# Performance work log

Measured on AMD Instinct MI355X. Metric: run time of the kernel, lower is better.

The kernel has to match this reference:

```python
import jax, jax.numpy as jnp
import numpy as np

N = 50000      # n_nodes
E = 800000     # n_edges
D = 64         # in_dim == out_dim
K = 3          # k-neighbourhoods {1,2,3} at t=2
T = 2          # layer index t
NU = 1         # cfg.nu -> delay(k) = max(k - nu, 0)
AGG_EPS = 1e-6
BN_EPS = 1e-5


def setup_inputs() -> dict:
    key = jax.random.key(0)
    ks = jax.random.split(key, 8)
    xs = jax.random.normal(ks[0], (T + 1, N, D), dtype=jnp.float32)
    edge_index = jax.random.randint(ks[1], (2, E), 0, N, dtype=jnp.int32)
    edge_attr = jax.random.randint(ks[2], (E,), 1, K + 1, dtype=jnp.int32)  # hop k in {1..K}
    s = 1.0 / np.sqrt(D)
    Wa = jax.random.normal(ks[3], (D, D), dtype=jnp.float32) * s
    Wd = jax.random.normal(ks[4], (D, D), dtype=jnp.float32) * s
    Wb = jax.random.normal(ks[5], (K, D, D), dtype=jnp.float32) * s
    return {
        "xs": xs,
        "edge_index": edge_index,
        "edge_attr": edge_attr,
        "Wa": Wa, "ba": jnp.zeros((D,), jnp.float32),
        "Wd": Wd, "bd": jnp.zeros((D,), jnp.float32),
        "Wb": Wb, "bb": jnp.zeros((K, D), jnp.float32),
        "gamma": jnp.ones((D,), jnp.float32),
        "beta": jnp.zeros((D,), jnp.float32),
    }


def reference(xs, edge_index, edge_attr, Wa, ba, Wd, bd, Wb, bb, gamma, beta):
    # current node state
    x = xs[T]  # [N, D]
    # delayed state per hop k: xs[t - max(k - nu, 0)] -> indices [2, 1, 0] for k = 1,2,3
    state_idx = jnp.array([T - max(k - NU, 0) for k in range(1, K + 1)])
    states = xs[state_idx]                                   # [K, N, D]
    # per-k linear B_k (source uses B for both Bx and Ex)
    Bx = jnp.einsum('knd,kdo->kno', states, Wb) + bb[:, None, :]  # [K, N, D]
    Ex = Bx
    Ax = x @ Wa + ba                                         # [N, D]
    Dx = x @ Wd + bd                                         # [N, D]

    i_idx = edge_index[1]                                    # destination
    j_idx = edge_index[0]                                    # source
    ke = edge_attr - 1                                       # [E], 0..K-1

    Dx_i = Dx[i_idx]                                         # [E, D]
    Ex_j = Ex[ke, j_idx]                                     # [E, D] per-k gather
    Bx_j = Bx[ke, j_idx]                                     # [E, D]

    sigma = jax.nn.sigmoid(Dx_i + Ex_j)                      # [E, D]

    # per-(node, k) scatter-sum; segment id packs (i, k)
    seg = i_idx * K + ke
    num = jax.ops.segment_sum(sigma * Bx_j, seg, num_segments=N * K).reshape(N, K, D)
    den = jax.ops.segment_sum(sigma, seg, num_segments=N * K).reshape(N, K, D)
    eta = num / (den + AGG_EPS)                              # [N, K, D]

    alpha = 1.0 / K  # softmax(ones(K)) with convex combination
    x_new = Ax + alpha * eta.sum(axis=1)                     # [N, D]

    # BatchNorm1d over nodes (training-mode batch statistics, biased var)
    mean = x_new.mean(axis=0)
    var = jnp.var(x_new, axis=0)
    y = gamma * (x_new - mean) * jax.lax.rsqrt(var + BN_EPS) + beta
    return jax.nn.relu(y)  # dropout p=0.0, residual=False
```

## Files before the change

### kernel.cpp

```cpp
#include <hip/hip_runtime.h>
#include <hip/hip_bf16.h>

#define D 64
#define K 3

typedef __hip_bfloat16 bf16;

__device__ __forceinline__ float b2f(bf16 v) { return __bfloat162float(v); }

__device__ __forceinline__ unsigned short f2bf(float f)
{
    const unsigned x = __float_as_uint(f);
    return (unsigned short)((x + 0x7FFFu + ((x >> 16) & 1u)) >> 16);
}

#define P_WA 0
#define P_BA 4096
#define P_WD 4160
#define P_BD 8256
#define P_WB 8320
#define P_BB 20608
#define P_G  20800
#define P_B  20864
#define P_TOTAL 20928

#define LOG2E 1.442695041f

#define NB_MAX 1024
#define BKN    128
#define BKSEG  (BKN * K)

__global__ void cvt_hist_kernel(const void* Wa, const void* ba, const void* Wd, const void* bd,
                                const void* Wb, const void* bb, const void* g, const void* b,
                                float* __restrict__ P, int* __restrict__ flag,
                                const int* __restrict__ ei,
                                int* __restrict__ bcnt, int E, int HB, int cb, int NB)
{
    __shared__ int bins[NB_MAX];
    const int bid = blockIdx.x;
    const int tid = threadIdx.x;

    if (bid < HB) {
        for (int i = tid; i < NB; i += 256) bins[i] = 0;
        __syncthreads();
        const int tstr = HB * 256;
        for (int e = bid * 256 + tid; e < E; e += tstr)
            atomicAdd(&bins[ei[E + e] >> 7], 1);
        __syncthreads();
        for (int i = tid; i < NB; i += 256) {
            const int c = bins[i];
            if (c) atomicAdd(&bcnt[i], c);
        }
        return;
    }

    const int isbf = (((const unsigned int*)g)[0] == 0x3F803F80u) ? 1 : 0;
    if (bid == HB && tid == 0) *flag = isbf;
    int i = (bid - HB) * 256 + tid;
    const int stride = cb * 256;
    for (; i < P_TOTAL; i += stride) {
        const void* src; int off;
        if (i < P_BA)      { src = Wa; off = i; }
        else if (i < P_WD) { src = ba; off = i - P_BA; }
        else if (i < P_BD) { src = Wd; off = i - P_WD; }
        else if (i < P_WB) { src = bd; off = i - P_BD; }
        else if (i < P_BB) { src = Wb; off = i - P_WB; }
        else if (i < P_G)  { src = bb; off = i - P_BB; }
        else if (i < P_B)  { src = g;  off = i - P_G; }
        else               { src = b;  off = i - P_B; }
        float v;
        if (isbf) v = b2f(((const bf16*)src)[off]);
        else      v = ((const float*)src)[off];
        P[i] = v;
    }
}

union U8 { float4 f; ushort4 u; };

__device__ __forceinline__ void lin_load(U8 reg[8], const void* xs_raw, size_t xbase,
                                         int isbf, int tid, int nbase, int N)
{
    if (isbf) {
        const ushort* xp = (const ushort*)xs_raw + xbase;
        #pragma unroll
        for (int p = 0; p < 8; p++) {
            const int idx = tid + (p << 8);
            const int n = nbase + (idx >> 4), c4 = (idx & 15) << 2;
            if (n < N) reg[p].u = *(const ushort4*)(xp + (size_t)n * D + c4);
            else       reg[p].u = make_ushort4(0, 0, 0, 0);
        }
    } else {
        const float* xp = (const float*)xs_raw + xbase;
        #pragma unroll
        for (int p = 0; p < 8; p++) {
            const int idx = tid + (p << 8);
            const int n = nbase + (idx >> 4), c4 = (idx & 15) << 2;
            if (n < N) reg[p].f = *(const float4*)(xp + (size_t)n * D + c4);
            else       reg[p].f = make_float4(0.f, 0.f, 0.f, 0.f);
        }
    }
}

__global__ void lin_scan_kernel(const void* __restrict__ xs_raw,
                                const float* __restrict__ P, const int* __restrict__ flag,
                                float* __restrict__ Ax, float* __restrict__ Dx,
                                void* __restrict__ Bx, int N,
                                const int* __restrict__ bcnt, int* __restrict__ bbase,
                                int* __restrict__ bcur, int* __restrict__ off,
                                int M, int E, int NB, int gx, int LB)
{
    __shared__ __align__(16) float sw[64][64];
    __shared__ float sx[128][65];
    __shared__ float sbias[64];
    __shared__ int sscan[256];

    const int bid = blockIdx.x;
    const int tid = threadIdx.x;

    if (bid >= LB) {
        const int base = tid * 4;
        int v[4];
        #pragma unroll
        for (int q = 0; q < 4; q++) {
            const int i = base + q;
            v[q] = (i < NB) ? bcnt[i] : 0;
        }
        const int tsum = v[0] + v[1] + v[2] + v[3];
        sscan[tid] = tsum;
        __syncthreads();
        #pragma unroll
        for (int o = 1; o < 256; o <<= 1) {
            int x = (tid >= o) ? sscan[tid - o] : 0;
            __syncthreads();
            sscan[tid] += x;
            __syncthreads();
        }
        int run = sscan[tid] - tsum;
        #pragma unroll
        for (int q = 0; q < 4; q++) {
            const int i = base + q;
            if (i < NB) { bbase[i] = run; bcur[i] = run; }
            run += v[q];
        }
        if (tid == 0) off[M] = E;
        return;
    }

    const int isbf = *flag;
    const int which = bid / gx;
    const int t0    = bid % gx;
    const size_t ND = (size_t)N * D;

    const float* W; const float* bias; size_t xbase;
    float* outf = nullptr; ushort* outh = nullptr;
    if (which == 0)      { W = P + P_WA; bias = P + P_BA; xbase = 2 * ND; outf = Ax; }
    else if (which == 1) { W = P + P_WD; bias = P + P_BD; xbase = 2 * ND; outf = Dx; }
    else {
        const int k = which - 2;
        W = P + P_WB + (size_t)k * D * D;
        bias = P + P_BB + (size_t)k * D;
        const int layer = 2 - k;
        xbase = (size_t)layer * ND;
        if (isbf) outh = (ushort*)Bx + k * ND;
        else      outf = (float*)Bx + k * ND;
    }
    const int bfout = (outh != nullptr);

    for (int idx = tid; idx < D * D; idx += 256)
        sw[idx >> 6][idx & 63] = W[idx];
    if (tid < 64) sbias[tid] = bias[tid];

    const int tiles = (N + 127) >> 7;

    U8 reg[8];
    int t = t0;
    if (t < tiles) lin_load(reg, xs_raw, xbase, isbf, tid, t << 7, N);

    const int ct = tid & 7;  const int c0 = ct * 8;
    const int nt = tid >> 3; const int n0 = nt * 4;

    for (; t < tiles; t += gx) {
        __syncthreads();
        #pragma unroll
        for (int p = 0; p < 8; p++) {
            const int idx = tid + (p << 8);
            const int n = idx >> 4, c4 = (idx & 15) << 2;
            float v0, v1, v2, v3;
            if (isbf) {
                v0 = __uint_as_float((unsigned)reg[p].u.x << 16);
                v1 = __uint_as_float((unsigned)reg[p].u.y << 16);
                v2 = __uint_as_float((unsigned)reg[p].u.z << 16);
                v3 = __uint_as_float((unsigned)reg[p].u.w << 16);
            } else {
                v0 = reg[p].f.x; v1 = reg[p].f.y; v2 = reg[p].f.z; v3 = reg[p].f.w;
            }
            sx[n][c4 + 0] = v0; sx[n][c4 + 1] = v1;
            sx[n][c4 + 2] = v2; sx[n][c4 + 3] = v3;
        }
        __syncthreads();

        const int tn = t + gx;
        if (tn < tiles) lin_load(reg, xs_raw, xbase, isbf, tid, tn << 7, N);

        float acc[4][8];
        {
            float b0[8];
            #pragma unroll
            for (int j = 0; j < 8; j++) b0[j] = sbias[c0 + j];
            #pragma unroll
            for (int i = 0; i < 4; i++)
                #pragma unroll
                for (int j = 0; j < 8; j++) acc[i][j] = b0[j];
        }

        #pragma unroll 8
        for (int kk = 0; kk < 64; kk++) {
            const float4 wlo = *(const float4*)&sw[kk][c0];
            const float4 whi = *(const float4*)&sw[kk][c0 + 4];
            float xv[4];
            #pragma unroll
            for (int i = 0; i < 4; i++) xv[i] = sx[n0 + i][kk];
            #pragma unroll
            for (int i = 0; i < 4; i++) {
                acc[i][0] += xv[i] * wlo.x; acc[i][1] += xv[i] * wlo.y;
                acc[i][2] += xv[i] * wlo.z; acc[i][3] += xv[i] * wlo.w;
                acc[i][4] += xv[i] * whi.x; acc[i][5] += xv[i] * whi.y;
                acc[i][6] += xv[i] * whi.z; acc[i][7] += xv[i] * whi.w;
            }
        }

        const int nbase = t << 7;
        #pragma unroll
        for (int i = 0; i < 4; i++) {
            const int gn = nbase + n0 + i;
            if (gn < N) {
                if (bfout) {
                    ushort* op = outh + (size_t)gn * D + c0;
                    *(ushort4*)op = make_ushort4(f2bf(acc[i][0]), f2bf(acc[i][1]),
                                                 f2bf(acc[i][2]), f2bf(acc[i][3]));
                    *(ushort4*)(op + 4) = make_ushort4(f2bf(acc[i][4]), f2bf(acc[i][5]),
                                                       f2bf(acc[i][6]), f2bf(acc[i][7]));
                } else {
                    float* op = outf + (size_t)gn * D + c0;
                    *(float4*)op       = make_float4(acc[i][0], acc[i][1], acc[i][2], acc[i][3]);
                    *(float4*)(op + 4) = make_float4(acc[i][4], acc[i][5], acc[i][6], acc[i][7]);
                }
            }
        }
    }
}

__global__ void binscat_kernel(const int* __restrict__ ei, const int* __restrict__ ea,
                               int* __restrict__ bcur, int* __restrict__ bkt,
                               int E, int NB, int CH)
{
    __shared__ int lcnt[NB_MAX];
    __shared__ int lbase[NB_MAX];
    const int bid = blockIdx.x, tid = threadIdx.x;
    const int s0 = bid * CH;
    int s1 = s0 + CH; if (s1 > E) s1 = E;

    for (int i = tid; i < NB; i += 256) lcnt[i] = 0;
    __syncthreads();
    for (int e = s0 + tid; e < s1; e += 256)
        atomicAdd(&lcnt[ei[E + e] >> 7], 1);
    __syncthreads();
    for (int b = tid; b < NB; b += 256) {
        const int c = lcnt[b];
        lbase[b] = c ? atomicAdd(&bcur[b], c) : 0;
        lcnt[b] = 0;
    }
    __syncthreads();
    for (int e = s0 + tid; e < s1; e += 256) {
        const int i  = ei[E + e];
        const int j  = ei[e];
        const int ke = ea[e] - 1;
        const int b  = i >> 7;
        const int r  = atomicAdd(&lcnt[b], 1);
        bkt[lbase[b] + r] = ((i & 127) << 19) | (ke << 17) | j;
    }
}

__global__ void bucketsort_kernel(const int* __restrict__ bbase, const int* __restrict__ bcur,
                                  const int* __restrict__ bkt,
                                  int* __restrict__ off, int* __restrict__ elist, int M)
{
    __shared__ int cl[512];
    __shared__ int cu[512];
    const int b = blockIdx.x, tid = threadIdx.x;
    const int s0 = bbase[b], s1 = bcur[b];

    cl[tid] = 0; cl[tid + 256] = 0;
    __syncthreads();
    for (int idx = s0 + tid; idx < s1; idx += 256) {
        const int p = bkt[idx];
        atomicAdd(&cl[(p >> 19) * 3 + ((p >> 17) & 3)], 1);
    }
    __syncthreads();
    const int c0 = cl[tid], c1 = cl[tid + 256];
    for (int o = 1; o < 512; o <<= 1) {
        const int a0 = (tid >= o) ? cl[tid - o] : 0;
        const int a1 = cl[tid + 256 - o];
        __syncthreads();
        cl[tid] += a0; cl[tid + 256] += a1;
        __syncthreads();
    }
    const int e0 = cl[tid] - c0, e1 = cl[tid + 256] - c1;
    cu[tid] = e0; cu[tid + 256] = e1;
    const int gbase = b * BKSEG;
    {
        const int gs0 = gbase + tid;
        if (tid < BKSEG && gs0 < M) off[gs0] = s0 + e0;
        const int ls1 = tid + 256;
        const int gs1 = gbase + ls1;
        if (ls1 < BKSEG && gs1 < M) off[gs1] = s0 + e1;
    }
    __syncthreads();
    for (int idx = s0 + tid; idx < s1; idx += 256) {
        const int p = bkt[idx];
        const int ls = (p >> 19) * 3 + ((p >> 17) & 3);
        const int pos = atomicAdd(&cu[ls], 1);
        elist[s0 + pos] = p & 0x1FFFF;
    }
}

template<int BF>
__device__ __forceinline__ float ldbx(const void* bxk, int j, int d)
{
    if (BF) {
        const ushort u = ((const ushort*)bxk)[((size_t)(unsigned)j << 6) + d];
        return __uint_as_float((unsigned)u << 16);
    }
    return ((const float*)bxk)[((size_t)(unsigned)j << 6) + d];
}

template<int BF>
__device__ __forceinline__ float node_eta(const void* __restrict__ Bx, size_t ND,
                                          const int* __restrict__ elist,
                                          int o0, int o1, int o2, int o3,
                                          int d, float ndx)
{
    int wb = o0;
    int jv = (wb + d < o3) ? elist[wb + d] : 0;
    float eta = 0.f;
    #pragma unroll
    for (int k = 0; k < K; k++) {
        const void* bxk = (const char*)Bx + (size_t)k * ND * (BF ? 2 : 4);
        const int sbeg = (k == 0) ? o0 : (k == 1) ? o1 : o2;
        const int send = (k == 0) ? o1 : (k == 1) ? o2 : o3;
        float num = 0.f, den = 0.f;
        int p = sbeg;
        while (p < send) {
            if (p - wb >= 64) {
                wb = p;
                jv = (wb + d < o3) ? elist[wb + d] : 0;
            }
            int lim = wb + 64; if (lim > send) lim = send;
            int c = p - wb;
            const int cend = lim - wb;
            for (; c + 3 < cend; c += 4) {
                const int j0 = __builtin_amdgcn_readlane(jv, c);
                const int j1 = __builtin_amdgcn_readlane(jv, c + 1);
                const int j2 = __builtin_amdgcn_readlane(jv, c + 2);
                const int j3 = __builtin_amdgcn_readlane(jv, c + 3);
                const float bx0 = ldbx<BF>(bxk, j0, d);
                const float bx1 = ldbx<BF>(bxk, j1, d);
                const float bx2 = ldbx<BF>(bxk, j2, d);
                const float bx3 = ldbx<BF>(bxk, j3, d);
                const float s0 = __builtin_amdgcn_rcpf(1.f + __builtin_amdgcn_exp2f(fmaf(bx0, -LOG2E, ndx)));
                const float s1 = __builtin_amdgcn_rcpf(1.f + __builtin_amdgcn_exp2f(fmaf(bx1, -LOG2E, ndx)));
                const float s2 = __builtin_amdgcn_rcpf(1.f + __builtin_amdgcn_exp2f(fmaf(bx2, -LOG2E, ndx)));
                const float s3 = __builtin_amdgcn_rcpf(1.f + __builtin_amdgcn_exp2f(fmaf(bx3, -LOG2E, ndx)));
                num = fmaf(s0, bx0, num); den += s0;
                num = fmaf(s1, bx1, num); den += s1;
                num = fmaf(s2, bx2, num); den += s2;
                num = fmaf(s3, bx3, num); den += s3;
            }
            for (; c < cend; ++c) {
                const int j0 = __builtin_amdgcn_readlane(jv, c);
                const float bx0 = ldbx<BF>(bxk, j0, d);
                const float s0 = __builtin_amdgcn_rcpf(1.f + __builtin_amdgcn_exp2f(fmaf(bx0, -LOG2E, ndx)));
                num = fmaf(s0, bx0, num); den += s0;
            }
            p = lim;
        }
        eta = fmaf(num, __builtin_amdgcn_rcpf(den + 1e-6f), eta);
    }
    return eta;
}

__global__ void node_kernel(float* __restrict__ Ax,
                            const float* __restrict__ Dx, const void* __restrict__ Bx,
                            const int* __restrict__ off, const int* __restrict__ elist,
                            float* __restrict__ statsP, const int* __restrict__ flag, int N)
{
    __shared__ float red[256];
    const int tid = threadIdx.x;
    const int w = tid >> 6, d = tid & 63;
    const size_t ND = (size_t)N * D;
    const int isbf = *flag;

    float lsum = 0.f, lsq = 0.f;
    for (int n = blockIdx.x * 4 + w; n < N; n += gridDim.x * 4) {
        const float dx = Dx[(size_t)n * D + d];
        const float ndx = dx * -LOG2E;
        const int b0 = n * 3;
        const int o0 = off[b0];
        const int o1 = off[b0 + 1];
        const int o2 = off[b0 + 2];
        const int o3 = off[b0 + 3];
        const float eta = isbf ? node_eta<1>(Bx, ND, elist, o0, o1, o2, o3, d, ndx)
                               : node_eta<0>(Bx, ND, elist, o0, o1, o2, o3, d, ndx);
        const size_t xi = (size_t)n * D + d;
        const float v = Ax[xi] + eta * (1.f / 3.f);
        Ax[xi] = v;
        lsum += v;
        lsq  += v * v;
    }

    red[tid] = lsum;
    __syncthreads();
    if (tid < 64) {
        float* sp = statsP + (size_t)(blockIdx.x & 63) * 128;
        atomicAdd(&sp[d], red[d] + red[64 + d] + red[128 + d] + red[192 + d]);
    }
    __syncthreads();
    red[tid] = lsq;
    __syncthreads();
    if (tid < 64) {
        float* sp = statsP + (size_t)(blockIdx.x & 63) * 128;
        atomicAdd(&sp[64 + d], red[d] + red[64 + d] + red[128 + d] + red[192 + d]);
    }
}

__global__ void bnreduce_kernel(const float* __restrict__ statsP, float* __restrict__ stats)
{
    const int t = threadIdx.x;
    float a = 0.f;
    for (int c = 0; c < 64; c++) a += statsP[c * 128 + t];
    stats[t] = a;
}

__global__ void finalize_kernel(const float* __restrict__ xnew, const float* __restrict__ stats,
                                const float* __restrict__ P, const int* __restrict__ flag,
                                void* __restrict__ out, int N)
{
    const long long g = (long long)blockIdx.x * blockDim.x + threadIdx.x;
    if (g >= (long long)N * D) return;
    const int d = (int)(g & 63);

    const float invN = 1.f / (float)N;
    const float mean = stats[d] * invN;
    const float var  = stats[64 + d] * invN - mean * mean;
    const float rstd = rsqrtf(var + 1e-5f);

    float y = P[P_G + d] * (xnew[g] - mean) * rstd + P[P_B + d];
    y = fmaxf(y, 0.f);

    if (*flag) ((bf16*)out)[g] = __float2bfloat16(y);
    else       ((float*)out)[g] = y;
}

extern "C" void kernel_launch(void* const* d_in, const int* in_sizes, int n_in,
                              void* d_out, int out_size, void* d_ws, size_t ws_size,
                              hipStream_t stream)
{
    const void* xs = d_in[0];
    const int*  ei = (const int*)d_in[1];
    const int*  ea = (const int*)d_in[2];

    const int N = in_sizes[0] / (3 * D);
    const int E = in_sizes[2];
    const int M = N * K;
    const int NB = (N + BKN - 1) / BKN;

    float* ws = (float*)d_ws;
    const size_t nd = (size_t)N * D;

    float* P      = ws;
    int*   flag   = (int*)(P + P_TOTAL);
    float* Ax     = (float*)(flag + 1);
    float* Dx     = Ax + nd;
    float* Bx     = Dx + nd;
    float* statsP = Bx + 3 * nd;
    float* stats  = statsP + 64 * 128;
    int*   bcnt   = (int*)(stats + 128);
    int*   bbase  = bcnt + NB_MAX;
    int*   bcur   = bbase + NB_MAX;
    int*   off    = bcur + NB_MAX;
    int*   bkt    = off + (M + 1);
    int*   elist  = bkt + E;

    const size_t zbytes = (size_t)(64 * 128 + 128 + NB_MAX) * 4;
    hipMemsetAsync(statsP, 0, zbytes, stream);

    const int HB = 128;
    const int cb = 82;
    cvt_hist_kernel<<<HB + cb, 256, 0, stream>>>(
        d_in[3], d_in[4], d_in[5], d_in[6], d_in[7], d_in[8], d_in[9], d_in[10],
        P, flag, ei, bcnt, E, HB, cb, NB);

    const int tiles = (N + 127) / 128;
    const int gx = (tiles < 144) ? tiles : 144;
    const int LB = gx * 5;
    lin_scan_kernel<<<LB + 1, 256, 0, stream>>>(xs, P, flag, Ax, Dx, (void*)Bx, N,
                                                bcnt, bbase, bcur, off, M, E, NB, gx, LB);

    const int HB2 = 128;
    const int CH = (E + HB2 - 1) / HB2;
    binscat_kernel<<<HB2, 256, 0, stream>>>(ei, ea, bcur, bkt, E, NB, CH);

    bucketsort_kernel<<<NB, 256, 0, stream>>>(bbase, bcur, bkt, off, elist, M);

    node_kernel<<<2048, 256, 0, stream>>>(Ax, Dx, (const void*)Bx, off, elist, statsP, flag, N);

    bnreduce_kernel<<<1, 128, 0, stream>>>(statsP, stats);

    finalize_kernel<<<(int)((nd + 255) / 256), 256, 0, stream>>>(Ax, stats, P, flag, d_out, N);
}
```

Baseline: 238.8 us.

## Fuse scan, bin-scatter and BN reduce into neighbouring kernels to cut launches

Moves the bucket prefix scan into the histogram kernel, run by the last-finishing block detected through an atomic done counter. Merges the bin-scatter pass into the linear-transform kernel as extra blocks so both run concurrently. Folds the BN partial-sum reduction into the tail of node_kernel through the same last-block pattern. This removes two kernel launches and the serial gaps between them, at the cost of threadfence/atomic last-block synchronisation and a larger shared-memory footprint that is now shared by both roles. The histogram block count also doubles.

```diff
diff --git a/kernel.cpp b/kernel.cpp
--- a/kernel.cpp
+++ b/kernel.cpp
@@ -34,9 +34,13 @@
                                 const void* Wb, const void* bb, const void* g, const void* b,
                                 float* __restrict__ P, int* __restrict__ flag,
                                 const int* __restrict__ ei,
-                                int* __restrict__ bcnt, int E, int HB, int cb, int NB)
+                                int* __restrict__ bcnt, int* __restrict__ bbase,
+                                int* __restrict__ bcur, int* __restrict__ off,
+                                int* __restrict__ done,
+                                int E, int M, int HB, int cb, int NB)
 {
     __shared__ int bins[NB_MAX];
+    __shared__ int lastret;
     const int bid = blockIdx.x;
     const int tid = threadIdx.x;
 
@@ -50,6 +54,38 @@
         for (int i = tid; i < NB; i += 256) {
             const int c = bins[i];
             if (c) atomicAdd(&bcnt[i], c);
+        }
+        __threadfence();
+        __syncthreads();
+        if (tid == 0) lastret = atomicAdd(done, 1);
+        __syncthreads();
+        if (lastret == HB - 1) {
+            __threadfence();
+            const int base = tid * 4;
+            int v[4];
+            #pragma unroll
+            for (int q = 0; q < 4; q++) {
+                const int i = base + q;
+                v[q] = (i < NB) ? bcnt[i] : 0;
+            }
+            const int tsum = v[0] + v[1] + v[2] + v[3];
+            bins[tid] = tsum;
+            __syncthreads();
+            #pragma unroll
+            for (int o = 1; o < 256; o <<= 1) {
+                int x = (tid >= o) ? bins[tid - o] : 0;
+                __syncthreads();
+                bins[tid] += x;
+                __syncthreads();
+            }
+            int run = bins[tid] - tsum;
+            #pragma unroll
+            for (int q = 0; q < 4; q++) {
+                const int i = base + q;
+                if (i < NB) { bbase[i] = run; bcur[i] = run; }
+                run += v[q];
+            }
+            if (tid == 0) off[M] = E;
         }
         return;
     }
@@ -59,18 +95,18 @@
     int i = (bid - HB) * 256 + tid;
     const int stride = cb * 256;
     for (; i < P_TOTAL; i += stride) {
-        const void* src; int off;
-        if (i < P_BA)      { src = Wa; off = i; }
-        else if (i < P_WD) { src = ba; off = i - P_BA; }
-        else if (i < P_BD) { src = Wd; off = i - P_WD; }
-        else if (i < P_WB) { src = bd; off = i - P_BD; }
-        else if (i < P_BB) { src = Wb; off = i - P_WB; }
-        else if (i < P_G)  { src = bb; off = i - P_BB; }
-        else if (i < P_B)  { src = g;  off = i - P_G; }
-        else               { src = b;  off = i - P_B; }
+        const void* src; int off_;
+        if (i < P_BA)      { src = Wa; off_ = i; }
+        else if (i < P_WD) { src = ba; off_ = i - P_BA; }
+        else if (i < P_BD) { src = Wd; off_ = i - P_WD; }
+        else if (i < P_WB) { src = bd; off_ = i - P_BD; }
+        else if (i < P_BB) { src = Wb; off_ = i - P_WB; }
+        else if (i < P_G)  { src = bb; off_ = i - P_BB; }
+        else if (i < P_B)  { src = g;  off_ = i - P_G; }
+        else               { src = b;  off_ = i - P_B; }
         float v;
-        if (isbf) v = b2f(((const bf16*)src)[off]);
-        else      v = ((const float*)src)[off];
+        if (isbf) v = b2f(((const bf16*)src)[off_]);
+        else      v = ((const float*)src)[off_];
         P[i] = v;
     }
 }
@@ -101,54 +137,54 @@
     }
 }
 
-__global__ void lin_scan_kernel(const void* __restrict__ xs_raw,
-                                const float* __restrict__ P, const int* __restrict__ flag,
-                                float* __restrict__ Ax, float* __restrict__ Dx,
-                                void* __restrict__ Bx, int N,
-                                const int* __restrict__ bcnt, int* __restrict__ bbase,
-                                int* __restrict__ bcur, int* __restrict__ off,
-                                int M, int E, int NB, int gx, int LB)
-{
-    __shared__ __align__(16) float sw[64][64];
-    __shared__ float sx[128][65];
-    __shared__ float sbias[64];
-    __shared__ int sscan[256];
-
+__global__ void lin_binscat_kernel(const void* __restrict__ xs_raw,
+                                   const float* __restrict__ P, const int* __restrict__ flag,
+                                   float* __restrict__ Ax, float* __restrict__ Dx,
+                                   void* __restrict__ Bx, int N,
+                                   const int* __restrict__ ei, const int* __restrict__ ea,
+                                   int* __restrict__ bcur, int* __restrict__ bkt,
+                                   int E, int NB, int CH, int SB, int gx)
+{
+    __shared__ __align__(16) char smem[49920];
     const int bid = blockIdx.x;
     const int tid = threadIdx.x;
 
-    if (bid >= LB) {
-        const int base = tid * 4;
-        int v[4];
-        #pragma unroll
-        for (int q = 0; q < 4; q++) {
-            const int i = base + q;
-            v[q] = (i < NB) ? bcnt[i] : 0;
-        }
-        const int tsum = v[0] + v[1] + v[2] + v[3];
-        sscan[tid] = tsum;
-        __syncthreads();
-        #pragma unroll
-        for (int o = 1; o < 256; o <<= 1) {
-            int x = (tid >= o) ? sscan[tid - o] : 0;
-            __syncthreads();
-            sscan[tid] += x;
-            __syncthreads();
-        }
-        int run = sscan[tid] - tsum;
-        #pragma unroll
-        for (int q = 0; q < 4; q++) {
-            const int i = base + q;
-            if (i < NB) { bbase[i] = run; bcur[i] = run; }
-            run += v[q];
-        }
-        if (tid == 0) off[M] = E;
+    if (bid < SB) {
+        int* lcnt  = (int*)smem;
+        int* lbase = (int*)(smem + 4096);
+        const int s0 = bid * CH;
+        int s1 = s0 + CH; if (s1 > E) s1 = E;
+
+        for (int i = tid; i < NB; i += 256) lcnt[i] = 0;
+        __syncthreads();
+        for (int e = s0 + tid; e < s1; e += 256)
+            atomicAdd(&lcnt[ei[E + e] >> 7], 1);
+        __syncthreads();
+        for (int b = tid; b < NB; b += 256) {
+            const int c = lcnt[b];
+            lbase[b] = c ? atomicAdd(&bcur[b], c) : 0;
+            lcnt[b] = 0;
+        }
+        __syncthreads();
+        for (int e = s0 + tid; e < s1; e += 256) {
+            const int i  = ei[E + e];
+            const int j  = ei[e];
+            const int ke = ea[e] - 1;
+            const int b  = i >> 7;
+            const int r  = atomicAdd(&lcnt[b], 1);
+            bkt[lbase[b] + r] = ((i & 127) << 19) | (ke << 17) | j;
+        }
         return;
     }
 
+    float (*sw)[64] = (float(*)[64])smem;
+    float (*sx)[65] = (float(*)[65])(smem + 16384);
+    float* sbias    = (float*)(smem + 49664);
+
     const int isbf = *flag;
-    const int which = bid / gx;
-    const int t0    = bid % gx;
+    const int lb = bid - SB;
+    const int which = lb / gx;
+    const int t0    = lb % gx;
     const size_t ND = (size_t)N * D;
 
     const float* W; const float* bias; size_t xbase;
@@ -247,37 +283,6 @@
                 }
             }
         }
-    }
-}
-
-__global__ void binscat_kernel(const int* __restrict__ ei, const int* __restrict__ ea,
-                               int* __restrict__ bcur, int* __restrict__ bkt,
-                               int E, int NB, int CH)
-{
-    __shared__ int lcnt[NB_MAX];
-    __shared__ int lbase[NB_MAX];
-    const int bid = blockIdx.x, tid = threadIdx.x;
-    const int s0 = bid * CH;
-    int s1 = s0 + CH; if (s1 > E) s1 = E;
-
-    for (int i = tid; i < NB; i += 256) lcnt[i] = 0;
-    __syncthreads();
-    for (int e = s0 + tid; e < s1; e += 256)
-        atomicAdd(&lcnt[ei[E + e] >> 7], 1);
-    __syncthreads();
-    for (int b = tid; b < NB; b += 256) {
-        const int c = lcnt[b];
-        lbase[b] = c ? atomicAdd(&bcur[b], c) : 0;
-        lcnt[b] = 0;
-    }
-    __syncthreads();
-    for (int e = s0 + tid; e < s1; e += 256) {
-        const int i  = ei[E + e];
-        const int j  = ei[e];
-        const int ke = ea[e] - 1;
-        const int b  = i >> 7;
-        const int r  = atomicAdd(&lcnt[b], 1);
-        bkt[lbase[b] + r] = ((i & 127) << 19) | (ke << 17) | j;
     }
 }
 
@@ -392,9 +397,11 @@
 __global__ void node_kernel(float* __restrict__ Ax,
                             const float* __restrict__ Dx, const void* __restrict__ Bx,
                             const int* __restrict__ off, const int* __restrict__ elist,
-                            float* __restrict__ statsP, const int* __restrict__ flag, int N)
+                            float* __restrict__ statsP, float* __restrict__ stats,
+                            int* __restrict__ done, const int* __restrict__ flag, int N)
 {
     __shared__ float red[256];
+    __shared__ int lastret;
     const int tid = threadIdx.x;
     const int w = tid >> 6, d = tid & 63;
     const size_t ND = (size_t)N * D;
@@ -431,14 +438,19 @@
         float* sp = statsP + (size_t)(blockIdx.x & 63) * 128;
         atomicAdd(&sp[64 + d], red[d] + red[64 + d] + red[128 + d] + red[192 + d]);
     }
-}
-
-__global__ void bnreduce_kernel(const float* __restrict__ statsP, float* __restrict__ stats)
-{
-    const int t = threadIdx.x;
-    float a = 0.f;
-    for (int c = 0; c < 64; c++) a += statsP[c * 128 + t];
-    stats[t] = a;
+
+    __threadfence();
+    __syncthreads();
+    if (tid == 0) lastret = atomicAdd(done, 1);
+    __syncthreads();
+    if (lastret == (int)gridDim.x - 1) {
+        __threadfence();
+        if (tid < 128) {
+            float a = 0.f;
+            for (int c = 0; c < 64; c++) a += statsP[c * 128 + tid];
+            stats[tid] = a;
+        }
+    }
 }
 
 __global__ void finalize_kernel(const float* __restrict__ xnew, const float* __restrict__ stats,
@@ -485,36 +497,34 @@
     float* statsP = Bx + 3 * nd;
     float* stats  = statsP + 64 * 128;
     int*   bcnt   = (int*)(stats + 128);
-    int*   bbase  = bcnt + NB_MAX;
+    int*   done   = bcnt + NB_MAX;
+    int*   bbase  = done + 2;
     int*   bcur   = bbase + NB_MAX;
     int*   off    = bcur + NB_MAX;
     int*   bkt    = off + (M + 1);
     int*   elist  = bkt + E;
 
-    const size_t zbytes = (size_t)(64 * 128 + 128 + NB_MAX) * 4;
+    const size_t zbytes = (size_t)(64 * 128 + 128 + NB_MAX + 2) * 4;
     hipMemsetAsync(statsP, 0, zbytes, stream);
 
-    const int HB = 128;
+    const int HB = 256;
     const int cb = 82;
     cvt_hist_kernel<<<HB + cb, 256, 0, stream>>>(
         d_in[3], d_in[4], d_in[5], d_in[6], d_in[7], d_in[8], d_in[9], d_in[10],
-        P, flag, ei, bcnt, E, HB, cb, NB);
+        P, flag, ei, bcnt, bbase, bcur, off, done, E, M, HB, cb, NB);
 
     const int tiles = (N + 127) / 128;
     const int gx = (tiles < 144) ? tiles : 144;
     const int LB = gx * 5;
-    lin_scan_kernel<<<LB + 1, 256, 0, stream>>>(xs, P, flag, Ax, Dx, (void*)Bx, N,
-                                                bcnt, bbase, bcur, off, M, E, NB, gx, LB);
-
-    const int HB2 = 128;
-    const int CH = (E + HB2 - 1) / HB2;
-    binscat_kernel<<<HB2, 256, 0, stream>>>(ei, ea, bcur, bkt, E, NB, CH);
+    const int SB = 128;
+    const int CH = (E + SB - 1) / SB;
+    lin_binscat_kernel<<<SB + LB, 256, 0, stream>>>(xs, P, flag, Ax, Dx, (void*)Bx, N,
+                                                    ei, ea, bcur, bkt, E, NB, CH, SB, gx);
 
     bucketsort_kernel<<<NB, 256, 0, stream>>>(bbase, bcur, bkt, off, elist, M);
 
-    node_kernel<<<2048, 256, 0, stream>>>(Ax, Dx, (const void*)Bx, off, elist, statsP, flag, N);
-
-    bnreduce_kernel<<<1, 128, 0, stream>>>(statsP, stats);
+    node_kernel<<<2048, 256, 0, stream>>>(Ax, Dx, (const void*)Bx, off, elist,
+                                          statsP, stats, done + 1, flag, N);
 
     finalize_kernel<<<(int)((nd + 255) / 256), 256, 0, stream>>>(Ax, stats, P, flag, d_out, N);
 }
```

After: 411.5 us. 72.3% more time.
